# Performance work log

Measured on AMD Instinct MI355X. Metric: run time of the kernel, lower is better.

## Reference

```python
import jax, jax.numpy as jnp
import numpy as np

DIM = 1024
NUM_HEADS = 16
HEAD_DIM = DIM // NUM_HEADS
B, L = 2, 2048


def setup_inputs() -> dict:
    key = jax.random.key(0)
    k_x, k_qkv, k_pw, k_pb = jax.random.split(key, 4)
    x = jax.random.normal(k_x, (B, L, DIM), dtype=jnp.float32)
    # nn.Linear(dim, 3*dim, bias=False): weight [3*dim, dim]; y = x @ W.T
    w_qkv = jax.random.normal(k_qkv, (3 * DIM, DIM), dtype=jnp.float32) * (DIM ** -0.5)
    # nn.Linear(dim, dim) with bias
    w_proj = jax.random.normal(k_pw, (DIM, DIM), dtype=jnp.float32) * (DIM ** -0.5)
    b_proj = jax.random.normal(k_pb, (DIM,), dtype=jnp.float32) * 0.01
    return {"x": x, "w_qkv": w_qkv, "w_proj": w_proj, "b_proj": b_proj}


def reference(x, w_qkv, w_proj, b_proj):
    Bx, Lx, C = x.shape
    qkv = x @ w_qkv.T  # [B, L, 3C]
    qkv = qkv.reshape(Bx, Lx, 3, NUM_HEADS, HEAD_DIM)
    q = jnp.transpose(qkv[:, :, 0], (0, 2, 1, 3))  # [B, H, L, D]
    k = jnp.transpose(qkv[:, :, 1], (0, 2, 1, 3))
    v = jnp.transpose(qkv[:, :, 2], (0, 2, 1, 3))
    attn = jnp.einsum('bhqd,bhkd->bhqk', q, k) * (HEAD_DIM ** -0.5)
    attn = jax.nn.softmax(attn, axis=-1)
    out = jnp.einsum('bhqk,bhkd->bhqd', attn, v)  # [B, H, L, D]
    out = jnp.transpose(out, (0, 2, 1, 3)).reshape(Bx, Lx, C)
    return out @ w_proj.T + b_proj
```

## Files before the change

### kernel.cpp

```cpp
#include <hip/hip_runtime.h>

#define DIM 1024
#define NH 16
#define HD 64
#define BB 2
#define LL 2048
#define BL (BB*LL)
#define NQKV (3*DIM)

typedef __bf16 bf16;
typedef __bf16 bf16x4 __attribute__((ext_vector_type(4)));
typedef __bf16 bf16x8 __attribute__((ext_vector_type(8)));
typedef float  f32x4  __attribute__((ext_vector_type(4)));

#define QSCALE 0.1803368801111204f

typedef __attribute__((address_space(3))) unsigned int lds_u32;
typedef __attribute__((address_space(1))) unsigned int glb_u32;

__device__ __forceinline__ void gld_lds16(const bf16* g, bf16* l) {
    __builtin_amdgcn_global_load_lds((const glb_u32*)g, (lds_u32*)l, 16, 0, 0);
}

#define C0 (BL*DIM/4)
#define C1 (NQKV*DIM/4)
#define C2 (DIM*DIM/4)
__global__ __launch_bounds__(256) void cvt_all(const float* __restrict__ x,
        const float* __restrict__ wq, const float* __restrict__ wp,
        bf16* __restrict__ xb, bf16* __restrict__ wqb, bf16* __restrict__ wpb) {
    int i = blockIdx.x * 256 + threadIdx.x;
    const float* in; bf16* out; int j;
    if (i < C0)            { in = x;  out = xb;  j = i; }
    else if (i < C0 + C1)  { in = wq; out = wqb; j = i - C0; }
    else                   { in = wp; out = wpb; j = i - C0 - C1; }
    float4 f = ((const float4*)in)[j];
    bf16x4 o = { (bf16)f.x, (bf16)f.y, (bf16)f.z, (bf16)f.w };
    ((bf16x4*)out)[j] = o;
}

__global__ __launch_bounds__(256, 3) void gemm_qkv(
        const bf16* __restrict__ A, const bf16* __restrict__ W,
        bf16* __restrict__ Qb, bf16* __restrict__ Kb, bf16* __restrict__ VTb) {
    __shared__ bf16 As[128][64];
    __shared__ bf16 Bs[128][64];
    const int tid = threadIdx.x;
    const int w = tid >> 6, lane = tid & 63, quad = lane >> 4, l16 = lane & 15;
    const int n0 = blockIdx.x * 128, m0 = blockIdx.y * 128;
    const int wm = (w & 1) * 64, wn = (w >> 1) * 64;
    f32x4 acc[4][4] = {};
    for (int k0 = 0; k0 < DIM; k0 += 64) {
        #pragma unroll
        for (int i = 0; i < 4; ++i) {
            int cb = w * 256 + i * 64;
            int gc = cb + lane;
            int r = gc >> 3;
            int cs = (gc & 7) ^ (r & 7);
            gld_lds16(A + (size_t)(m0 + r) * DIM + k0 + cs*8, &As[0][0] + cb * 8);
            gld_lds16(W + (size_t)(n0 + r) * DIM + k0 + cs*8, &Bs[0][0] + cb * 8);
        }
        __syncthreads();
        #pragma unroll
        for (int kc = 0; kc < 2; ++kc) {
            bf16x8 af[4], bfr[4];
            #pragma unroll
            for (int t = 0; t < 4; ++t) {
                int rw = wn + t*16 + l16;
                int cw = (kc*4 + quad) ^ (rw & 7);
                af[t] = *(const bf16x8*)(&Bs[0][0] + rw*64 + cw*8);
                int rx = wm + t*16 + l16;
                int cx = (kc*4 + quad) ^ (rx & 7);
                bfr[t] = *(const bf16x8*)(&As[0][0] + rx*64 + cx*8);
            }
            #pragma unroll
            for (int tm = 0; tm < 4; ++tm)
                #pragma unroll
                for (int tn = 0; tn < 4; ++tn)
                    acc[tm][tn] = __builtin_amdgcn_mfma_f32_16x16x32_bf16(
                                      af[tm], bfr[tn], acc[tm][tn], 0, 0, 0);
        }
        __syncthreads();
    }
    const int which = n0 >> 10;
    #pragma unroll
    for (int tm = 0; tm < 4; ++tm) {
        int nb = n0 + wn + tm*16 + quad*4;
        int rem = nb & 1023, h = rem >> 6, db = rem & 63;
        #pragma unroll
        for (int tn = 0; tn < 4; ++tn) {
            int m = m0 + wm + tn*16 + l16;
            int b = m >> 11, l = m & 2047, bh = (b << 4) | h;
            if (which == 0) {
                bf16x4 q4 = { (bf16)(acc[tm][tn][0] * QSCALE),
                              (bf16)(acc[tm][tn][1] * QSCALE),
                              (bf16)(acc[tm][tn][2] * QSCALE),
                              (bf16)(acc[tm][tn][3] * QSCALE) };
                *(bf16x4*)(Qb + ((size_t)bh << 17) + ((size_t)l << 6) + db) = q4;
            } else if (which == 1) {
                bf16x4 k4 = { (bf16)acc[tm][tn][0], (bf16)acc[tm][tn][1],
                              (bf16)acc[tm][tn][2], (bf16)acc[tm][tn][3] };
                *(bf16x4*)(Kb + ((size_t)bh << 17) + ((size_t)l << 6) + db) = k4;
            } else {
                #pragma unroll
                for (int r = 0; r < 4; ++r)
                    VTb[((size_t)bh << 17) + ((size_t)(db + r) << 11) + l] =
                        (bf16)acc[tm][tn][r];
            }
        }
    }
}

__global__ __launch_bounds__(256, 3) void gemm_proj(
        const bf16* __restrict__ A, const bf16* __restrict__ W,
        const float* __restrict__ bias, float* __restrict__ out) {
    __shared__ bf16 As[128][64];
    __shared__ bf16 Bs[64][64];
    const int tid = threadIdx.x;
    const int w = tid >> 6, lane = tid & 63, quad = lane >> 4, l16 = lane & 15;
    const int n0 = blockIdx.x * 64, m0 = blockIdx.y * 128;
    const int wm = (w & 1) * 64, wn = (w >> 1) * 32;
    f32x4 acc[2][4] = {};
    for (int k0 = 0; k0 < DIM; k0 += 64) {
        #pragma unroll
        for (int i = 0; i < 4; ++i) {
            int cb = w * 256 + i * 64;
            int gc = cb + lane;
            int r = gc >> 3;
            int cs = (gc & 7) ^ (r & 7);
            gld_lds16(A + (size_t)(m0 + r) * DIM + k0 + cs*8, &As[0][0] + cb * 8);
        }
        #pragma unroll
        for (int i = 0; i < 2; ++i) {
            int cb = w * 128 + i * 64;
            int gc = cb + lane;
            int r = gc >> 3;
            int cs = (gc & 7) ^ (r & 7);
            gld_lds16(W + (size_t)(n0 + r) * DIM + k0 + cs*8, &Bs[0][0] + cb * 8);
        }
        __syncthreads();
        #pragma unroll
        for (int kc = 0; kc < 2; ++kc) {
            bf16x8 af[2], bfr[4];
            #pragma unroll
            for (int t = 0; t < 2; ++t) {
                int rw = wn + t*16 + l16;
                int cw = (kc*4 + quad) ^ (rw & 7);
                af[t] = *(const bf16x8*)(&Bs[0][0] + rw*64 + cw*8);
            }
            #pragma unroll
            for (int t = 0; t < 4; ++t) {
                int rx = wm + t*16 + l16;
                int cx = (kc*4 + quad) ^ (rx & 7);
                bfr[t] = *(const bf16x8*)(&As[0][0] + rx*64 + cx*8);
            }
            #pragma unroll
            for (int tm = 0; tm < 2; ++tm)
                #pragma unroll
                for (int tn = 0; tn < 4; ++tn)
                    acc[tm][tn] = __builtin_amdgcn_mfma_f32_16x16x32_bf16(
                                      af[tm], bfr[tn], acc[tm][tn], 0, 0, 0);
        }
        __syncthreads();
    }
    #pragma unroll
    for (int tm = 0; tm < 2; ++tm) {
        int nb = n0 + wn + tm*16 + quad*4;
        float4 b4 = *(const float4*)&bias[nb];
        #pragma unroll
        for (int tn = 0; tn < 4; ++tn) {
            int m = m0 + wm + tn*16 + l16;
            float4 o4 = { acc[tm][tn][0] + b4.x, acc[tm][tn][1] + b4.y,
                          acc[tm][tn][2] + b4.z, acc[tm][tn][3] + b4.w };
            *(float4*)(out + (size_t)m * DIM + nb) = o4;
        }
    }
}

__global__ __launch_bounds__(512, 2) void attn(
        const bf16* __restrict__ Qb, const bf16* __restrict__ Kb,
        const bf16* __restrict__ VTb, bf16* __restrict__ AO) {
    __shared__ __align__(16) char smem[33280];
    bf16* KsP  = (bf16*)smem;
    bf16* VTsP = KsP + 8192;
    const int tid = threadIdx.x;
    const int w = tid >> 6, lane = tid & 63, quad = lane >> 4, l16 = lane & 15;
    const int qw = w & 3, kvh = w >> 2;
    const int linear = blockIdx.y * 8 + blockIdx.x;
    const int swz = (linear & 7) * 32 + (linear >> 3);
    const int qt = swz & 7, bh = swz >> 3;
    const bf16* Qg = Qb + ((size_t)bh << 17) + (size_t)(qt * 256) * 64;
    const bf16* Kg = Kb + ((size_t)bh << 17);
    const bf16* Vg = VTb + ((size_t)bh << 17);

    bf16x8 aq[4][2];
    #pragma unroll
    for (int sub = 0; sub < 4; ++sub)
        #pragma unroll
        for (int kd = 0; kd < 2; ++kd)
            aq[sub][kd] = *(const bf16x8*)(Qg + (size_t)(qw*64 + sub*16 + l16) * 64
                                           + kd*32 + quad*8);

    bf16x8 onesf = {};
    if (l16 == 0)
        #pragma unroll
        for (int j = 0; j < 8; ++j) onesf[j] = (bf16)1.0f;

    f32x4 oacc[4][4] = {};
    f32x4 lacc[4] = {};
    const f32x4 zero4 = {};
    bf16x8 ap[4];

    auto stageK = [&](int kt, int buf) {
        int r = tid >> 3;
        int cs = (tid & 7) ^ (r & 7) ^ ((r >> 3) & 7) ^ ((r & 1) << 2);
        gld_lds16(Kg + (size_t)(kt*64 + r) * 64 + cs*8, KsP + buf*4096 + tid*8);
    };
    auto stageV = [&](int kt, int buf) {
        int r = tid >> 3;
        int cs = (tid & 7) ^ (r & 7) ^ ((r >> 3) & 7);
        gld_lds16(Vg + (size_t)r * 2048 + kt*64 + cs*8, VTsP + buf*4096 + tid*8);
    };
    auto pv = [&](int pbuf) {
        __builtin_amdgcn_s_setprio(1);
        #pragma unroll
        for (int nt = 0; nt < 4; ++nt) {
            int row = nt*16 + l16;
            int cp = (kvh*4 + quad) ^ (row & 7) ^ ((row >> 3) & 7);
            bf16x8 bv = *(const bf16x8*)(VTsP + pbuf*4096 + row*64 + cp*8);
            #pragma unroll
            for (int sub = 0; sub < 4; ++sub)
                oacc[sub][nt] = __builtin_amdgcn_mfma_f32_16x16x32_bf16(
                                    ap[sub], bv, oacc[sub][nt], 0, 0, 0);
        }
        #pragma unroll
        for (int sub = 0; sub < 4; ++sub)
            lacc[sub] = __builtin_amdgcn_mfma_f32_16x16x32_bf16(
                            ap[sub], onesf, lacc[sub], 0, 0, 0);
        __builtin_amdgcn_s_setprio(0);
    };

    auto body = [&](int kt, int cur) {
        __syncthreads();
        if (kt < 31) stageK(kt + 1, cur ^ 1);
        stageV(kt, cur);

        if (kt > 0) pv(cur ^ 1);

        f32x4 s[4][2];
        __builtin_amdgcn_s_setprio(1);
        #pragma unroll
        for (int u = 0; u < 2; ++u) {
            bf16x8 kf0, kf1;
            int rk = kvh*32 + ((l16 >> 2) << 3) + u*4 + (l16 & 3);
            int f = (rk & 7) ^ ((rk >> 3) & 7) ^ ((rk & 1) << 2);
            kf0 = *(const bf16x8*)(KsP + cur*4096 + rk*64 + ((0*4 + quad) ^ f)*8);
            kf1 = *(const bf16x8*)(KsP + cur*4096 + rk*64 + ((1*4 + quad) ^ f)*8);
            #pragma unroll
            for (int sub = 0; sub < 4; ++sub) {
                s[sub][u] = __builtin_amdgcn_mfma_f32_16x16x32_bf16(
                                kf0, aq[sub][0], zero4, 0, 0, 0);
                s[sub][u] = __builtin_amdgcn_mfma_f32_16x16x32_bf16(
                                kf1, aq[sub][1], s[sub][u], 0, 0, 0);
            }
        }
        __builtin_amdgcn_s_setprio(0);

        #pragma unroll
        for (int sub = 0; sub < 4; ++sub) {
            bf16x8 p;
            #pragma unroll
            for (int u = 0; u < 2; ++u)
                #pragma unroll
                for (int r = 0; r < 4; ++r)
                    p[u*4 + r] = (bf16)__builtin_amdgcn_exp2f(s[sub][u][r]);
            ap[sub] = p;
        }
    };

    stageK(0, 0);
    for (int kt2 = 0; kt2 < 32; kt2 += 2) {
        body(kt2,     0);
        body(kt2 + 1, 1);
    }
    __syncthreads();
    pv(1);

    float* OredF = (float*)smem;
    float* LredF = (float*)(smem + 32768);
    const int b = bh >> 4, h = bh & 15;
    #pragma unroll
    for (int t = 0; t < 2; ++t) {
        __syncthreads();
        if (kvh == 1 && (qw >> 1) == t) {
            int slot = qw & 1;
            #pragma unroll
            for (int sub = 0; sub < 4; ++sub)
                #pragma unroll
                for (int nt = 0; nt < 4; ++nt)
                    #pragma unroll
                    for (int r = 0; r < 4; ++r)
                        OredF[((slot*4 + sub)*16 + quad*4 + r)*64 + nt*16 + l16]
                            = oacc[sub][nt][r];
            if (l16 == 0)
                #pragma unroll
                for (int sub = 0; sub < 4; ++sub)
                    #pragma unroll
                    for (int r = 0; r < 4; ++r)
                        LredF[(slot*4 + sub)*16 + quad*4 + r] = lacc[sub][r];
        }
        __syncthreads();
        if (kvh == 0 && (qw >> 1) == t) {
            int slot = qw & 1;
            #pragma unroll
            for (int sub = 0; sub < 4; ++sub)
                #pragma unroll
                for (int nt = 0; nt < 4; ++nt)
                    #pragma unroll
                    for (int r = 0; r < 4; ++r)
                        oacc[sub][nt][r] +=
                            OredF[((slot*4 + sub)*16 + quad*4 + r)*64 + nt*16 + l16];
            if (l16 == 0)
                #pragma unroll
                for (int sub = 0; sub < 4; ++sub)
                    #pragma unroll
                    for (int r = 0; r < 4; ++r)
                        lacc[sub][r] += LredF[(slot*4 + sub)*16 + quad*4 + r];
            #pragma unroll
            for (int sub = 0; sub < 4; ++sub)
                #pragma unroll
                for (int r = 0; r < 4; ++r) {
                    float l = __shfl(lacc[sub][r], quad * 16, 64);
                    float inv = 1.0f / l;
                    int lq = qt*256 + qw*64 + sub*16 + quad*4 + r;
                    size_t rowbase = ((size_t)(b * 2048 + lq)) * DIM + h * 64;
                    #pragma unroll
                    for (int nt = 0; nt < 4; ++nt)
                        AO[rowbase + nt*16 + l16] = (bf16)(oacc[sub][nt][r] * inv);
                }
        }
    }
}

extern "C" void kernel_launch(void* const* d_in, const int* in_sizes, int n_in,
                              void* d_out, int out_size, void* d_ws, size_t ws_size,
                              hipStream_t stream) {
    const float* x      = (const float*)d_in[0];
    const float* w_qkv  = (const float*)d_in[1];
    const float* w_proj = (const float*)d_in[2];
    const float* b_proj = (const float*)d_in[3];
    float* out = (float*)d_out;
    char* ws = (char*)d_ws;

    bf16* xb  = (bf16*)(ws);
    bf16* wqb = (bf16*)(ws + ( 8u << 20));
    bf16* wpb = (bf16*)(ws + (14u << 20));
    bf16* Qb  = (bf16*)(ws + (16u << 20));
    bf16* Kb  = (bf16*)(ws + (24u << 20));
    bf16* VTb = (bf16*)(ws + (32u << 20));
    bf16* AOb = (bf16*)(ws + (40u << 20));

    cvt_all<<<(C0 + C1 + C2) / 256, 256, 0, stream>>>(x, w_qkv, w_proj, xb, wqb, wpb);
    gemm_qkv<<<dim3(NQKV/128, BL/128), 256, 0, stream>>>(xb, wqb, Qb, Kb, VTb);
    attn<<<dim3(LL/256, BB*NH),        512, 0, stream>>>(Qb, Kb, VTb, AOb);
    gemm_proj<<<dim3(DIM/64, BL/128),  256, 0, stream>>>(AOb, wpb, b_proj, out);
}
```

Before: 166.7 us.

## Double-buffer proj GEMM and widen attention KV tiles to 128 keys

The projection GEMM now double-buffers its A and W LDS tiles, prefetching the next K-slice while computing the current one, which removes one barrier per iteration. The attention kernel processes 128 keys per iteration instead of 64, with each KV-half wave group owning its own 64-key subtile, which halves the loop trip count and barrier count. The cost is doubled LDS (about 66KB per attention block, with 2 blocks per CU requested) and more live registers for scores and probabilities, which may reduce occupancy or cause spills.

```diff
diff --git a/kernel.cpp b/kernel.cpp
--- a/kernel.cpp
+++ b/kernel.cpp
@@ -112,21 +112,23 @@
 __global__ __launch_bounds__(256, 3) void gemm_proj(
         const bf16* __restrict__ A, const bf16* __restrict__ W,
         const float* __restrict__ bias, float* __restrict__ out) {
-    __shared__ bf16 As[128][64];
-    __shared__ bf16 Bs[64][64];
+    __shared__ bf16 As[2][128][64];
+    __shared__ bf16 Bs[2][64][64];
     const int tid = threadIdx.x;
     const int w = tid >> 6, lane = tid & 63, quad = lane >> 4, l16 = lane & 15;
     const int n0 = blockIdx.x * 64, m0 = blockIdx.y * 128;
     const int wm = (w & 1) * 64, wn = (w >> 1) * 32;
     f32x4 acc[2][4] = {};
-    for (int k0 = 0; k0 < DIM; k0 += 64) {
+
+    auto stage = [&](int k0, int buf) {
         #pragma unroll
         for (int i = 0; i < 4; ++i) {
             int cb = w * 256 + i * 64;
             int gc = cb + lane;
             int r = gc >> 3;
             int cs = (gc & 7) ^ (r & 7);
-            gld_lds16(A + (size_t)(m0 + r) * DIM + k0 + cs*8, &As[0][0] + cb * 8);
+            gld_lds16(A + (size_t)(m0 + r) * DIM + k0 + cs*8,
+                      &As[buf][0][0] + cb * 8);
         }
         #pragma unroll
         for (int i = 0; i < 2; ++i) {
@@ -134,9 +136,16 @@
             int gc = cb + lane;
             int r = gc >> 3;
             int cs = (gc & 7) ^ (r & 7);
-            gld_lds16(W + (size_t)(n0 + r) * DIM + k0 + cs*8, &Bs[0][0] + cb * 8);
-        }
-        __syncthreads();
+            gld_lds16(W + (size_t)(n0 + r) * DIM + k0 + cs*8,
+                      &Bs[buf][0][0] + cb * 8);
+        }
+    };
+
+    stage(0, 0);
+    for (int ks = 0; ks < 16; ++ks) {
+        const int cur = ks & 1;
+        __syncthreads();
+        if (ks < 15) stage((ks + 1) * 64, cur ^ 1);
         #pragma unroll
         for (int kc = 0; kc < 2; ++kc) {
             bf16x8 af[2], bfr[4];
@@ -144,13 +153,13 @@
             for (int t = 0; t < 2; ++t) {
                 int rw = wn + t*16 + l16;
                 int cw = (kc*4 + quad) ^ (rw & 7);
-                af[t] = *(const bf16x8*)(&Bs[0][0] + rw*64 + cw*8);
+                af[t] = *(const bf16x8*)(&Bs[cur][0][0] + rw*64 + cw*8);
             }
             #pragma unroll
             for (int t = 0; t < 4; ++t) {
                 int rx = wm + t*16 + l16;
                 int cx = (kc*4 + quad) ^ (rx & 7);
-                bfr[t] = *(const bf16x8*)(&As[0][0] + rx*64 + cx*8);
+                bfr[t] = *(const bf16x8*)(&As[cur][0][0] + rx*64 + cx*8);
             }
             #pragma unroll
             for (int tm = 0; tm < 2; ++tm)
@@ -159,7 +168,6 @@
                     acc[tm][tn] = __builtin_amdgcn_mfma_f32_16x16x32_bf16(
                                       af[tm], bfr[tn], acc[tm][tn], 0, 0, 0);
         }
-        __syncthreads();
     }
     #pragma unroll
     for (int tm = 0; tm < 2; ++tm) {
@@ -178,9 +186,9 @@
 __global__ __launch_bounds__(512, 2) void attn(
         const bf16* __restrict__ Qb, const bf16* __restrict__ Kb,
         const bf16* __restrict__ VTb, bf16* __restrict__ AO) {
-    __shared__ __align__(16) char smem[33280];
+    __shared__ __align__(16) char smem[66048];
     bf16* KsP  = (bf16*)smem;
-    bf16* VTsP = KsP + 8192;
+    bf16* VTsP = (bf16*)(smem + 32768);
     const int tid = threadIdx.x;
     const int w = tid >> 6, lane = tid & 63, quad = lane >> 4, l16 = lane & 15;
     const int qw = w & 3, kvh = w >> 2;
@@ -207,77 +215,93 @@
     f32x4 oacc[4][4] = {};
     f32x4 lacc[4] = {};
     const f32x4 zero4 = {};
-    bf16x8 ap[4];
+    bf16x8 ap[4][2];
 
     auto stageK = [&](int kt, int buf) {
-        int r = tid >> 3;
-        int cs = (tid & 7) ^ (r & 7) ^ ((r >> 3) & 7) ^ ((r & 1) << 2);
-        gld_lds16(Kg + (size_t)(kt*64 + r) * 64 + cs*8, KsP + buf*4096 + tid*8);
+        #pragma unroll
+        for (int sub = 0; sub < 2; ++sub) {
+            int r = tid >> 3;
+            int cs = (tid & 7) ^ (r & 7) ^ ((r >> 3) & 7) ^ ((r & 1) << 2);
+            gld_lds16(Kg + (size_t)(kt*128 + sub*64 + r) * 64 + cs*8,
+                      KsP + (buf*2 + sub) * 4096 + tid*8);
+        }
     };
     auto stageV = [&](int kt, int buf) {
-        int r = tid >> 3;
-        int cs = (tid & 7) ^ (r & 7) ^ ((r >> 3) & 7);
-        gld_lds16(Vg + (size_t)r * 2048 + kt*64 + cs*8, VTsP + buf*4096 + tid*8);
+        #pragma unroll
+        for (int sub = 0; sub < 2; ++sub) {
+            int r = tid >> 3;
+            int cs = (tid & 7) ^ (r & 7) ^ ((r >> 3) & 7);
+            gld_lds16(Vg + (size_t)r * 2048 + kt*128 + sub*64 + cs*8,
+                      VTsP + (buf*2 + sub) * 4096 + tid*8);
+        }
     };
     auto pv = [&](int pbuf) {
         __builtin_amdgcn_s_setprio(1);
         #pragma unroll
-        for (int nt = 0; nt < 4; ++nt) {
-            int row = nt*16 + l16;
-            int cp = (kvh*4 + quad) ^ (row & 7) ^ ((row >> 3) & 7);
-            bf16x8 bv = *(const bf16x8*)(VTsP + pbuf*4096 + row*64 + cp*8);
+        for (int kk = 0; kk < 2; ++kk) {
+            #pragma unroll
+            for (int nt = 0; nt < 4; ++nt) {
+                int row = nt*16 + l16;
+                int cp = (kk*4 + quad) ^ (row & 7) ^ ((row >> 3) & 7);
+                bf16x8 bv = *(const bf16x8*)(VTsP + (pbuf*2 + kvh) * 4096
+                                             + row*64 + cp*8);
+                #pragma unroll
+                for (int sub = 0; sub < 4; ++sub)
+                    oacc[sub][nt] = __builtin_amdgcn_mfma_f32_16x16x32_bf16(
+                                        ap[sub][kk], bv, oacc[sub][nt], 0, 0, 0);
+            }
             #pragma unroll
             for (int sub = 0; sub < 4; ++sub)
-                oacc[sub][nt] = __builtin_amdgcn_mfma_f32_16x16x32_bf16(
-                                    ap[sub], bv, oacc[sub][nt], 0, 0, 0);
-        }
+                lacc[sub] = __builtin_amdgcn_mfma_f32_16x16x32_bf16(
+                                ap[sub][kk], onesf, lacc[sub], 0, 0, 0);
+        }
+        __builtin_amdgcn_s_setprio(0);
+    };
+
+    auto body = [&](int kt, int cur) {
+        __syncthreads();
+        if (kt < 15) stageK(kt + 1, cur ^ 1);
+        stageV(kt, cur);
+
+        if (kt > 0) pv(cur ^ 1);
+
+        f32x4 s[4][2][2];
+        __builtin_amdgcn_s_setprio(1);
+        #pragma unroll
+        for (int kk = 0; kk < 2; ++kk)
+            #pragma unroll
+            for (int u = 0; u < 2; ++u) {
+                int rk = kk*32 + ((l16 >> 2) << 3) + u*4 + (l16 & 3);
+                int f = (rk & 7) ^ ((rk >> 3) & 7) ^ ((rk & 1) << 2);
+                const bf16* kb = KsP + (cur*2 + kvh) * 4096 + rk*64;
+                bf16x8 kf0 = *(const bf16x8*)(kb + ((0*4 + quad) ^ f)*8);
+                bf16x8 kf1 = *(const bf16x8*)(kb + ((1*4 + quad) ^ f)*8);
+                #pragma unroll
+                for (int sub = 0; sub < 4; ++sub) {
+                    s[sub][kk][u] = __builtin_amdgcn_mfma_f32_16x16x32_bf16(
+                                        kf0, aq[sub][0], zero4, 0, 0, 0);
+                    s[sub][kk][u] = __builtin_amdgcn_mfma_f32_16x16x32_bf16(
+                                        kf1, aq[sub][1], s[sub][kk][u], 0, 0, 0);
+                }
+            }
+        __builtin_amdgcn_s_setprio(0);
+
         #pragma unroll
         for (int sub = 0; sub < 4; ++sub)
-            lacc[sub] = __builtin_amdgcn_mfma_f32_16x16x32_bf16(
-                            ap[sub], onesf, lacc[sub], 0, 0, 0);
-        __builtin_amdgcn_s_setprio(0);
-    };
-
-    auto body = [&](int kt, int cur) {
-        __syncthreads();
-        if (kt < 31) stageK(kt + 1, cur ^ 1);
-        stageV(kt, cur);
-
-        if (kt > 0) pv(cur ^ 1);
-
-        f32x4 s[4][2];
-        __builtin_amdgcn_s_setprio(1);
-        #pragma unroll
-        for (int u = 0; u < 2; ++u) {
-            bf16x8 kf0, kf1;
-            int rk = kvh*32 + ((l16 >> 2) << 3) + u*4 + (l16 & 3);
-            int f = (rk & 7) ^ ((rk >> 3) & 7) ^ ((rk & 1) << 2);
-            kf0 = *(const bf16x8*)(KsP + cur*4096 + rk*64 + ((0*4 + quad) ^ f)*8);
-            kf1 = *(const bf16x8*)(KsP + cur*4096 + rk*64 + ((1*4 + quad) ^ f)*8);
-            #pragma unroll
-            for (int sub = 0; sub < 4; ++sub) {
-                s[sub][u] = __builtin_amdgcn_mfma_f32_16x16x32_bf16(
-                                kf0, aq[sub][0], zero4, 0, 0, 0);
-                s[sub][u] = __builtin_amdgcn_mfma_f32_16x16x32_bf16(
-                                kf1, aq[sub][1], s[sub][u], 0, 0, 0);
-            }
-        }
-        __builtin_amdgcn_s_setprio(0);
-
-        #pragma unroll
-        for (int sub = 0; sub < 4; ++sub) {
-            bf16x8 p;
-            #pragma unroll
-            for (int u = 0; u < 2; ++u)
-                #pragma unroll
-                for (int r = 0; r < 4; ++r)
-                    p[u*4 + r] = (bf16)__builtin_amdgcn_exp2f(s[sub][u][r]);
-            ap[sub] = p;
-        }
+            #pragma unroll
+            for (int kk = 0; kk < 2; ++kk) {
+                bf16x8 p;
+                #pragma unroll
+                for (int u = 0; u < 2; ++u)
+                    #pragma unroll
+                    for (int r = 0; r < 4; ++r)
+                        p[u*4 + r] = (bf16)__builtin_amdgcn_exp2f(s[sub][kk][u][r]);
+                ap[sub][kk] = p;
+            }
     };
 
     stageK(0, 0);
-    for (int kt2 = 0; kt2 < 32; kt2 += 2) {
+    for (int kt2 = 0; kt2 < 16; kt2 += 2) {
         body(kt2,     0);
         body(kt2 + 1, 1);
     }
```

After: 166.5 us (median of 2 runs). Within noise of the previous version (-0.1%).
